# Kernel optimization log

Measured on AMD Instinct MI355X. Metric: run time of the kernel, lower is better.

## Reference

```python
import jax, jax.numpy as jnp
import numpy as np

LN_EPS = 1e-5
MIN_BW, MAX_BW, BW_FACTOR = 0.1, 10.0, 1.0
BETA = 0.1


def _layernorm(h, g, b):
    mu = jnp.mean(h, axis=-1, keepdims=True)
    var = jnp.mean((h - mu) ** 2, axis=-1, keepdims=True)
    return (h - mu) * jax.lax.rsqrt(var + LN_EPS) * g + b


def _mlp(x, W1, b1, g, beta, W2, b2):
    # Linear -> LayerNorm -> Dropout(eval: identity) -> GELU(exact) -> Linear
    h = x @ W1 + b1
    h = _layernorm(h, g, beta)
    h = jax.nn.gelu(h, approximate=False)
    return h @ W2 + b2


def _normalize(x):
    n = jnp.linalg.norm(x, axis=-1, keepdims=True)
    return x / jnp.maximum(n, 1e-12)


def _bandwidth(x, y):
    # median-heuristic bandwidth on up to 512 samples; no grad through it
    s = min(512, x.shape[0])
    xs, ys = x[:s], y[:s]
    diff = xs[:, None, :] - ys[None, :, :]          # [s, s, K]
    dist_sq = jnp.sum(diff ** 2, axis=-1)
    bw = jnp.sqrt(jnp.median(dist_sq.reshape(-1)) / 2.0) * BW_FACTOR
    return jax.lax.stop_gradient(jnp.clip(bw, MIN_BW, MAX_BW))


def _score_kernel(x, sx, y, sy):
    # 3-term KSD kernel matrix [B, B]
    bw = _bandwidth(x, y)
    bw2 = bw ** 2
    x2 = jnp.sum(x ** 2, axis=-1)
    y2 = jnp.sum(y ** 2, axis=-1)
    dist_sq = jnp.maximum(x2[:, None] + y2[None, :] - 2.0 * (x @ y.T), 0.0)
    k = jnp.exp(-dist_sq / (2.0 * bw2))
    term1 = k * (sx @ sy.T)
    # sum_d (x_i - y_j)_d * sy_jd  = x_i . sy_j - y_j . sy_j
    term2 = (x @ sy.T - jnp.sum(y * sy, axis=-1)[None, :]) * k / bw2
    D = x.shape[-1]
    term3 = dist_sq * k / (bw2 ** 2) - k * D / bw2
    return term1 + term2 + term3


def setup_inputs() -> dict:
    key = jax.random.key(0)
    B, L, D1, H, K = 256, 128, 768, 1024, 256
    ks = jax.random.split(key, 16)

    def w(k, shape):
        return (jax.random.normal(k, shape, dtype=jnp.float32) * 0.02)

    inp = {
        'image_features': jax.random.normal(ks[0], (B, L, D1), dtype=jnp.float32),
        'text_features': jax.random.normal(ks[1], (B, L, D1), dtype=jnp.float32),
        'eps_img': jax.random.normal(ks[2], (B, L, K), dtype=jnp.float32),
        'eps_txt': jax.random.normal(ks[3], (B, L, K), dtype=jnp.float32),
        'attention_mask': jnp.ones((B, L), dtype=jnp.int32),
    }
    # encoders: D1 -> H -> 2K ; score nets: K -> 2K -> K
    for pfx, k1, k2 in (('enc_i', ks[4], ks[5]), ('enc_t', ks[6], ks[7])):
        inp[pfx + '_W1'] = w(k1, (D1, H)); inp[pfx + '_b1'] = jnp.zeros((H,), jnp.float32)
        inp[pfx + '_g'] = jnp.ones((H,), jnp.float32); inp[pfx + '_beta'] = jnp.zeros((H,), jnp.float32)
        inp[pfx + '_W2'] = w(k2, (H, 2 * K)); inp[pfx + '_b2'] = jnp.zeros((2 * K,), jnp.float32)
    for pfx, k1, k2 in (('sc_i', ks[8], ks[9]), ('sc_t', ks[10], ks[11])):
        inp[pfx + '_W1'] = w(k1, (K, 2 * K)); inp[pfx + '_b1'] = jnp.zeros((2 * K,), jnp.float32)
        inp[pfx + '_g'] = jnp.ones((2 * K,), jnp.float32); inp[pfx + '_beta'] = jnp.zeros((2 * K,), jnp.float32)
        inp[pfx + '_W2'] = w(k2, (2 * K, K)); inp[pfx + '_b2'] = jnp.zeros((K,), jnp.float32)
    return inp


def reference(image_features, text_features, attention_mask, eps_img, eps_txt,
              enc_i_W1, enc_i_b1, enc_i_g, enc_i_beta, enc_i_W2, enc_i_b2,
              enc_t_W1, enc_t_b1, enc_t_g, enc_t_beta, enc_t_W2, enc_t_b2,
              sc_i_W1, sc_i_b1, sc_i_g, sc_i_beta, sc_i_W2, sc_i_b2,
              sc_t_W1, sc_t_b1, sc_t_g, sc_t_beta, sc_t_W2, sc_t_b2):
    B = image_features.shape[0]
    img_params = _mlp(image_features, enc_i_W1, enc_i_b1, enc_i_g, enc_i_beta, enc_i_W2, enc_i_b2)
    txt_params = _mlp(text_features, enc_t_W1, enc_t_b1, enc_t_g, enc_t_beta, enc_t_W2, enc_t_b2)
    K = img_params.shape[-1] // 2
    img_mu, img_logvar = img_params[..., :K], img_params[..., K:]
    txt_mu, txt_logvar = txt_params[..., :K], txt_params[..., K:]

    img_z = _normalize(img_mu + eps_img * jnp.exp(0.5 * img_logvar))
    txt_z = _normalize(txt_mu + eps_txt * jnp.exp(0.5 * txt_logvar))

    img_score = _mlp(img_z, sc_i_W1, sc_i_b1, sc_i_g, sc_i_beta, sc_i_W2, sc_i_b2)
    txt_score = _mlp(txt_z, sc_t_W1, sc_t_b1, sc_t_g, sc_t_beta, sc_t_W2, sc_t_b2)

    seq_last = jnp.sum(attention_mask, axis=1).astype(jnp.int32) - 1   # [B]
    bidx = jnp.arange(B)
    xz, yz = img_z[bidx, seq_last], txt_z[bidx, seq_last]
    xs, ys = img_score[bidx, seq_last], txt_score[bidx, seq_last]

    alignment_loss = jnp.mean(_score_kernel(xz, xs, yz, ys))

    kl1 = -0.5 * jnp.sum(1.0 + img_logvar - img_mu ** 2 - jnp.exp(img_logvar), axis=-1)
    kl2 = -0.5 * jnp.sum(1.0 + txt_logvar - txt_mu ** 2 - jnp.exp(txt_logvar), axis=-1)
    kl_loss = (jnp.mean(kl1[bidx, seq_last]) + jnp.mean(kl2[bidx, seq_last])) / 2.0

    total_loss = kl_loss + BETA * alignment_loss
    return total_loss
```

## Files before the change

kernel.cpp:

```cpp
#include <hip/hip_runtime.h>
#include <math.h>

#define Bb   256
#define Lq   128
#define D1   768
#define Hh   1024
#define Kk   256
#define K2v  512

#define OFF_EPSG  0
#define OFF_H1    131072
#define OFF_H2    655360
#define OFF_H3    917504
#define OFF_Z     1179648
#define OFF_SCORE 1310720
#define OFF_DIST  1441792
#define OFF_HIST  1507328
#define OFF_SCAL  1515520
#define OFF_YSY   1515528
#define OFF_BF    1516048

#define UB_XG   0
#define UB_WT   393216
#define WT_EW1I 0
#define WT_EW1T 786432
#define WT_EW2I 1572864
#define WT_EW2T 2097152
#define WT_SW1I 2621440
#define WT_SW1T 2752512
#define WT_SW2I 2883584
#define WT_SW2T 3014656

typedef __attribute__((ext_vector_type(8))) short short8v;
typedef __attribute__((ext_vector_type(4))) float f32x4;

__device__ __forceinline__ float wred(float v){
#pragma unroll
  for (int m = 32; m; m >>= 1) v += __shfl_xor(v, m, 64);
  return v;
}
__device__ __forceinline__ int wredi(int v){
#pragma unroll
  for (int m = 32; m; m >>= 1) v += __shfl_xor(v, m, 64);
  return v;
}
__device__ __forceinline__ float gelu_exact(float x){
  return 0.5f * x * (1.0f + erff(x * 0.70710678118654752f));
}
__device__ __forceinline__ ushort f2b(float f){
  union { float f; unsigned u; } v; v.f = f;
  return (ushort)((v.u + 0x7FFFu + ((v.u >> 16) & 1u)) >> 16);
}
__device__ __forceinline__ int swzq(int k8, int m){
  return ((k8 >> 2)*16 + m)*64 + ((((k8 & 3) << 4)) ^ ((m & 3) << 4));
}
__device__ __forceinline__ int swzr(int ks, int l15, int kg){
  return (ks*16 + l15)*64 + ((kg*16) ^ ((l15 & 3) << 4));
}

__device__ __forceinline__ void wconv64(
    const float* __restrict__ src, ushort* __restrict__ dst,
    int Kd, int Nd, int ti, int t, float (*lsf)[65])
{
  const int ntile = Nd >> 6;
  const int k0 = (ti / ntile) << 6, n0 = (ti % ntile) << 6;
  const int r = t >> 2, c4 = t & 3;
  const float4* s4 = reinterpret_cast<const float4*>(src + (size_t)(k0 + r) * Nd + n0);
#pragma unroll
  for (int j = 0; j < 4; j++){
    float4 v = s4[c4 * 4 + j];
    lsf[r][c4*16 + j*4 + 0] = v.x;
    lsf[r][c4*16 + j*4 + 1] = v.y;
    lsf[r][c4*16 + j*4 + 2] = v.z;
    lsf[r][c4*16 + j*4 + 3] = v.w;
  }
  __syncthreads();
  ushort* d = dst + (size_t)(n0 + r) * Kd + k0 + c4 * 16;
#pragma unroll
  for (int h = 0; h < 2; h++){
    short8v o;
#pragma unroll
    for (int j = 0; j < 8; j++) o[j] = (short)f2b(lsf[c4*16 + h*8 + j][r]);
    *reinterpret_cast<short8v*>(d + h*8) = o;
  }
}

__global__ __launch_bounds__(256) void k_prep(
    const float* __restrict__ img, const float* __restrict__ txt,
    const float* __restrict__ epsi, const float* __restrict__ epst,
    const int* __restrict__ mask,
    const float* __restrict__ eW1i, const float* __restrict__ eW1t,
    ushort* __restrict__ xgb, float* __restrict__ epsg, ushort* __restrict__ wt,
    int* __restrict__ ghist, float* __restrict__ scal, float* __restrict__ ysy)
{
  __shared__ __align__(16) float lsf[64][65];
  __shared__ int s_last;
  const int bid = blockIdx.x, t = threadIdx.x;
  if (bid < 256){
    if (t < 8) reinterpret_cast<int4*>(ghist)[bid * 8 + t] = make_int4(0,0,0,0);
    if (bid == 0 && t < 8) scal[t] = 0.0f;
    if (t < 2) ysy[bid * 2 + t] = 0.0f;
    int s = 0;
    if (t < 32){
      int4 v = reinterpret_cast<const int4*>(mask + bid * Lq)[t];
      s = v.x + v.y + v.z + v.w;
    }
    if (t < 64){
      int tot = wredi(s);
      if (t == 0) s_last = tot - 1;
    }
    __syncthreads();
    const int last = s_last;
    if (t < 192){
      float4 v = reinterpret_cast<const float4*>(img + (size_t)(bid*Lq+last)*D1)[t];
      ushort4 o; o.x=f2b(v.x); o.y=f2b(v.y); o.z=f2b(v.z); o.w=f2b(v.w);
      reinterpret_cast<ushort4*>(xgb + (size_t)bid*D1)[t] = o;
      float4 w = reinterpret_cast<const float4*>(txt + (size_t)(bid*Lq+last)*D1)[t];
      ushort4 q; q.x=f2b(w.x); q.y=f2b(w.y); q.z=f2b(w.z); q.w=f2b(w.w);
      reinterpret_cast<ushort4*>(xgb + (size_t)(Bb+bid)*D1)[t] = q;
    }
    if (t < 64){
      reinterpret_cast<float4*>(epsg + (size_t)bid*Kk)[t] =
        reinterpret_cast<const float4*>(epsi + (size_t)(bid*Lq+last)*Kk)[t];
      reinterpret_cast<float4*>(epsg + (size_t)(Bb+bid)*Kk)[t] =
        reinterpret_cast<const float4*>(epst + (size_t)(bid*Lq+last)*Kk)[t];
    }
    return;
  }
  const int wb = bid - 256;
  if (wb < 192) wconv64(eW1i, wt + WT_EW1I, D1, Hh, wb, t, lsf);
  else          wconv64(eW1t, wt + WT_EW1T, D1, Hh, wb - 192, t, lsf);
}

__global__ __launch_bounds__(256) void k_enc1(
    const ushort* __restrict__ xgb,
    const ushort* __restrict__ WTi, const ushort* __restrict__ WTt,
    const float* __restrict__ b1i, const float* __restrict__ b1t,
    const float* __restrict__ eW2i, const float* __restrict__ eW2t,
    ushort* __restrict__ wt, float* __restrict__ H1)
{
  __shared__ __align__(16) char SM[16 * 768 * 2];
  const int bid = blockIdx.x, tid = threadIdx.x;
  if (bid >= 512){
    float (*lsf)[65] = reinterpret_cast<float(*)[65]>(SM);
    const int wb = bid - 512;
    if (wb < 128) wconv64(eW2i, wt + WT_EW2I, Hh, K2v, wb, tid, lsf);
    else          wconv64(eW2t, wt + WT_EW2T, Hh, K2v, wb - 128, tid, lsf);
    return;
  }
  char* ALS = SM;
  const int lane = tid & 63, w = tid >> 6;
  const int r0 = (bid >> 4) * 16, colbase = (bid & 15) * 64;
  const ushort* WT = (r0 >= 256) ? WTt : WTi;
  const float* b1 = (r0 >= 256) ? b1t : b1i;
  const int l15 = lane & 15, kg = lane >> 4;
  const int col = colbase + w*16 + l15;

  short8v areg[6];
  int mA[6], kA[6];
#pragma unroll
  for (int i = 0; i < 6; i++){
    const int q = i*256 + tid;
    mA[i] = q / 96; kA[i] = q % 96;
    areg[i] = *reinterpret_cast<const short8v*>(xgb + (size_t)(r0+mA[i])*D1 + kA[i]*8);
  }
  short8v breg[24];
  const ushort* wp = WT + (size_t)col*D1 + kg*8;
#pragma unroll
  for (int ks = 0; ks < 24; ks++)
    breg[ks] = *reinterpret_cast<const short8v*>(wp + ks*32);
#pragma unroll
  for (int i = 0; i < 6; i++)
    *reinterpret_cast<short8v*>(ALS + swzq(kA[i], mA[i])) = areg[i];
  __syncthreads();
  f32x4 acc = (f32x4){0.f,0.f,0.f,0.f};
#pragma unroll
  for (int ks = 0; ks < 24; ks++){
    short8v av = *reinterpret_cast<const short8v*>(ALS + swzr(ks, l15, kg));
    acc = __builtin_amdgcn_mfma_f32_16x16x32_bf16(av, breg[ks], acc, 0, 0, 0);
  }
  const float bias = b1[col];
#pragma unroll
  for (int r = 0; r < 4; r++)
    H1[(size_t)(r0 + kg*4 + r) * Hh + col] = acc[r] + bias;
}

__global__ __launch_bounds__(512) void k_enc2(
    const float* __restrict__ H1,
    const ushort* __restrict__ WTi, const ushort* __restrict__ WTt,
    const float* __restrict__ gi,  const float* __restrict__ gt,
    const float* __restrict__ bei, const float* __restrict__ bet,
    const float* __restrict__ b2i, const float* __restrict__ b2t,
    const float* __restrict__ sW1i, const float* __restrict__ sW1t,
    const float* __restrict__ sW2i, const float* __restrict__ sW2t,
    ushort* __restrict__ wt, float* __restrict__ H2)
{
  __shared__ __align__(16) char SM[16 * 1024 * 2];
  __shared__ __align__(16) float Rf[4][64][4];
  const int bid = blockIdx.x, tid = threadIdx.x;
  if (bid >= 256){
    if (tid < 256){
      float (*lsf)[65] = reinterpret_cast<float(*)[65]>(SM);
      const int wb = bid - 256;
      if      (wb < 32)  wconv64(sW1i, wt + WT_SW1I, Kk,  K2v, wb,      tid, lsf);
      else if (wb < 64)  wconv64(sW1t, wt + WT_SW1T, Kk,  K2v, wb - 32, tid, lsf);
      else if (wb < 96)  wconv64(sW2i, wt + WT_SW2I, K2v, Kk,  wb - 64, tid, lsf);
      else               wconv64(sW2t, wt + WT_SW2T, K2v, Kk,  wb - 96, tid, lsf);
    }
    return;
  }
  char* ALS = SM;
  const int lane = tid & 63, w = tid >> 6;
  const int r0 = (bid >> 3) * 16, colbase = (bid & 7) * 64;
  const ushort* WT = (r0 >= 256) ? WTt : WTi;
  const float* g  = (r0 >= 256) ? gt  : gi;
  const float* be = (r0 >= 256) ? bet : bei;
  const float* b2 = (r0 >= 256) ? b2t : b2i;
  const int l15 = lane & 15, kg = lane >> 4;
  const int ct = w & 3, khalf = w >> 2;
  const int col = colbase + ct*16 + l15;

  short8v breg[16];
  const ushort* wp = WT + (size_t)col*Hh + khalf*512 + kg*8;
#pragma unroll
  for (int i = 0; i < 16; i++)
    breg[i] = *reinterpret_cast<const short8v*>(wp + i*32);

#pragma unroll
  for (int rr = 0; rr < 2; rr++){
    const int row = w + rr*8, grow = r0 + row;
    const float4* h4 = reinterpret_cast<const float4*>(H1 + (size_t)grow * Hh);
    float4 v0 = h4[lane*4+0], v1 = h4[lane*4+1], v2 = h4[lane*4+2], v3 = h4[lane*4+3];
    float s = v0.x+v0.y+v0.z+v0.w + v1.x+v1.y+v1.z+v1.w
            + v2.x+v2.y+v2.z+v2.w + v3.x+v3.y+v3.z+v3.w;
    float q2 = v0.x*v0.x+v0.y*v0.y+v0.z*v0.z+v0.w*v0.w
             + v1.x*v1.x+v1.y*v1.y+v1.z*v1.z+v1.w*v1.w
             + v2.x*v2.x+v2.y*v2.y+v2.z*v2.z+v2.w*v2.w
             + v3.x*v3.x+v3.y*v3.y+v3.z*v3.z+v3.w*v3.w;
    s = wred(s); q2 = wred(q2);
    const float mean = s * (1.0f/1024.0f);
    const float rstd = rsqrtf(q2 * (1.0f/1024.0f) - mean*mean + 1e-5f);
    const float4* g4  = reinterpret_cast<const float4*>(g);
    const float4* be4 = reinterpret_cast<const float4*>(be);
    float hv[16] = {v0.x,v0.y,v0.z,v0.w, v1.x,v1.y,v1.z,v1.w,
                    v2.x,v2.y,v2.z,v2.w, v3.x,v3.y,v3.z,v3.w};
    short8v o0, o1;
#pragma unroll
    for (int j = 0; j < 16; j++){
      float4 gg = g4[lane*4 + (j>>2)];
      float4 bb = be4[lane*4 + (j>>2)];
      const float gs = (j&3)==0?gg.x:((j&3)==1?gg.y:((j&3)==2?gg.z:gg.w));
      const float bs = (j&3)==0?bb.x:((j&3)==1?bb.y:((j&3)==2?bb.z:bb.w));
      float x = gelu_exact((hv[j] - mean)*rstd*gs + bs);
      if (j < 8) o0[j] = (short)f2b(x); else o1[j-8] = (short)f2b(x);
    }
    *reinterpret_cast<short8v*>(ALS + swzq(lane*2,   row)) = o0;
    *reinterpret_cast<short8v*>(ALS + swzq(lane*2+1, row)) = o1;
  }
  __syncthreads();
  f32x4 acc = (f32x4){0.f,0.f,0.f,0.f};
#pragma unroll
  for (int i = 0; i < 16; i++){
    const int ks = khalf*16 + i;
    short8v av = *reinterpret_cast<const short8v*>(ALS + swzr(ks, l15, kg));
    acc = __builtin_amdgcn_mfma_f32_16x16x32_bf16(av, breg[i], acc, 0, 0, 0);
  }
  if (khalf) *reinterpret_cast<float4*>(&Rf[ct][lane][0]) = make_float4(acc[0],acc[1],acc[2],acc[3]);
  __syncthreads();
  if (!khalf){
    float4 o = *reinterpret_cast<const float4*>(&Rf[ct][lane][0]);
    const float bias = b2[col];
    H2[(size_t)(r0 + kg*4 + 0) * K2v + col] = acc[0]+o.x+bias;
    H2[(size_t)(r0 + kg*4 + 1) * K2v + col] = acc[1]+o.y+bias;
    H2[(size_t)(r0 + kg*4 + 2) * K2v + col] = acc[2]+o.z+bias;
    H2[(size_t)(r0 + kg*4 + 3) * K2v + col] = acc[3]+o.w+bias;
  }
}

__global__ __launch_bounds__(256) void k_sc1(
    const float* __restrict__ H2,
    const float* __restrict__ b2i, const float* __restrict__ b2t,
    const float* __restrict__ epsg,
    const ushort* __restrict__ W1i, const ushort* __restrict__ W1t,
    const float* __restrict__ sb1i, const float* __restrict__ sb1t,
    float* __restrict__ z, float* __restrict__ kl, float* __restrict__ H3)
{
  __shared__ __align__(16) char ALS[16 * 256 * 2];
  const int tid = threadIdx.x, lane = tid & 63, w = tid >> 6;
  const int r0 = blockIdx.y * 16, colblk = blockIdx.x, colbase = colblk * 64;
  const float* b2 = (r0 >= 256) ? b2t : b2i;
  const ushort* W1 = (r0 >= 256) ? W1t : W1i;
  const float* sb1 = (r0 >= 256) ? sb1t : sb1i;
  const int l15 = lane & 15, kg = lane >> 4;
  const int col = colbase + w*16 + l15;

  short8v breg[8];
  const ushort* wp = W1 + (size_t)col*Kk + kg*8;
#pragma unroll
  for (int ks = 0; ks < 8; ks++)
    breg[ks] = *reinterpret_cast<const short8v*>(wp + ks*32);

#pragma unroll
  for (int rr = 0; rr < 4; rr++){
    const int row = w + rr*4, grow = r0 + row;
    const float4* h4 = reinterpret_cast<const float4*>(H2 + (size_t)grow * K2v);
    float4 mu = h4[lane], lv = h4[64 + lane];
    float4 bm = reinterpret_cast<const float4*>(b2)[lane];
    float4 bl = reinterpret_cast<const float4*>(b2)[64 + lane];
    mu.x += bm.x; mu.y += bm.y; mu.z += bm.z; mu.w += bm.w;
    lv.x += bl.x; lv.y += bl.y; lv.z += bl.z; lv.w += bl.w;
    float4 ev = reinterpret_cast<const float4*>(epsg)[(size_t)grow * 64 + lane];
    float z0 = mu.x + ev.x * expf(0.5f * lv.x);
    float z1 = mu.y + ev.y * expf(0.5f * lv.y);
    float z2 = mu.z + ev.z * expf(0.5f * lv.z);
    float z3 = mu.w + ev.w * expf(0.5f * lv.w);
    float s2 = wred(z0*z0 + z1*z1 + z2*z2 + z3*z3);
    float klp = (1.0f + lv.x - mu.x*mu.x - expf(lv.x))
              + (1.0f + lv.y - mu.y*mu.y - expf(lv.y))
              + (1.0f + lv.z - mu.z*mu.z - expf(lv.z))
              + (1.0f + lv.w - mu.w*mu.w - expf(lv.w));
    float klt = wred(klp);
    float inv = 1.0f / fmaxf(sqrtf(s2), 1e-12f);
    float4 zv = make_float4(z0*inv, z1*inv, z2*inv, z3*inv);
    if (colblk == 0){
      reinterpret_cast<float4*>(z)[(size_t)grow * 64 + lane] = zv;
      if (lane == 0) atomicAdd(kl + (grow >= 256 ? 1 : 0), -0.5f * klt);
    }
    ushort4 o; o.x=f2b(zv.x); o.y=f2b(zv.y); o.z=f2b(zv.z); o.w=f2b(zv.w);
    *reinterpret_cast<ushort4*>(ALS + swzq(lane >> 1, row) + (lane & 1)*8) = o;
  }
  __syncthreads();
  f32x4 acc = (f32x4){0.f,0.f,0.f,0.f};
#pragma unroll
  for (int ks = 0; ks < 8; ks++){
    short8v av = *reinterpret_cast<const short8v*>(ALS + swzr(ks, l15, kg));
    acc = __builtin_amdgcn_mfma_f32_16x16x32_bf16(av, breg[ks], acc, 0, 0, 0);
  }
  const float bias = sb1[col];
#pragma unroll
  for (int r = 0; r < 4; r++)
    H3[(size_t)(r0 + kg*4 + r) * K2v + col] = acc[r] + bias;
}

__global__ __launch_bounds__(256) void k_sc2(
    const float* __restrict__ H3,
    const float* __restrict__ sgi,  const float* __restrict__ sgt,
    const float* __restrict__ sbei, const float* __restrict__ sbet,
    const ushort* __restrict__ W2i, const ushort* __restrict__ W2t,
    const float* __restrict__ sb2i, const float* __restrict__ sb2t,
    const float* __restrict__ z, float* __restrict__ score, float* __restrict__ ysy,
    float* __restrict__ dist, int* __restrict__ ghist)
{
  __shared__ __align__(16) char SM[33792];
  const int bid = blockIdx.x, tid = threadIdx.x;
  if (bid < 128){
    char* ALS = SM;
    const int lane = tid & 63, w = tid >> 6;
    const int r0 = (bid >> 2) * 16, colbase = (bid & 3) * 64;
    const float* g  = (r0 >= 256) ? sgt  : sgi;
    const float* be = (r0 >= 256) ? sbet : sbei;
    const ushort* W2 = (r0 >= 256) ? W2t : W2i;
    const float* b2 = (r0 >= 256) ? sb2t : sb2i;
    const int l15 = lane & 15, kg = lane >> 4;
    const int col = colbase + w*16 + l15;

    short8v breg[16];
    const ushort* wp = W2 + (size_t)col*K2v + kg*8;
#pragma unroll
    for (int ks = 0; ks < 16; ks++)
      breg[ks] = *reinterpret_cast<const short8v*>(wp + ks*32);

#pragma unroll
    for (int rr = 0; rr < 4; rr++){
      const int row = w + rr*4, grow = r0 + row;
      const float4* h4 = reinterpret_cast<const float4*>(H3 + (size_t)grow * K2v);
      float4 a = h4[lane*2], b = h4[lane*2+1];
      float s = a.x+a.y+a.z+a.w + b.x+b.y+b.z+b.w;
      float q2 = a.x*a.x+a.y*a.y+a.z*a.z+a.w*a.w + b.x*b.x+b.y*b.y+b.z*b.z+b.w*b.w;
      s = wred(s); q2 = wred(q2);
      const float mean = s * (1.0f/512.0f);
      const float rstd = rsqrtf(q2 * (1.0f/512.0f) - mean*mean + 1e-5f);
      float4 g0 = reinterpret_cast<const float4*>(g)[lane*2];
      float4 g1 = reinterpret_cast<const float4*>(g)[lane*2+1];
      float4 e0 = reinterpret_cast<const float4*>(be)[lane*2];
      float4 e1 = reinterpret_cast<const float4*>(be)[lane*2+1];
      short8v o;
      o[0] = (short)f2b(gelu_exact((a.x-mean)*rstd*g0.x + e0.x));
      o[1] = (short)f2b(gelu_exact((a.y-mean)*rstd*g0.y + e0.y));
      o[2] = (short)f2b(gelu_exact((a.z-mean)*rstd*g0.z + e0.z));
      o[3] = (short)f2b(gelu_exact((a.w-mean)*rstd*g0.w + e0.w));
      o[4] = (short)f2b(gelu_exact((b.x-mean)*rstd*g1.x + e1.x));
      o[5] = (short)f2b(gelu_exact((b.y-mean)*rstd*g1.y + e1.y));
      o[6] = (short)f2b(gelu_exact((b.z-mean)*rstd*g1.z + e1.z));
      o[7] = (short)f2b(gelu_exact((b.w-mean)*rstd*g1.w + e1.w));
      *reinterpret_cast<short8v*>(ALS + swzq(lane, row)) = o;
    }
    __syncthreads();
    f32x4 acc = (f32x4){0.f,0.f,0.f,0.f};
#pragma unroll
    for (int ks = 0; ks < 16; ks++){
      short8v av = *reinterpret_cast<const short8v*>(ALS + swzr(ks, l15, kg));
      acc = __builtin_amdgcn_mfma_f32_16x16x32_bf16(av, breg[ks], acc, 0, 0, 0);
    }
    const float bias = b2[col];
    float part[4];
#pragma unroll
    for (int r = 0; r < 4; r++){
      const int grow = r0 + kg*4 + r;
      const float sv = acc[r] + bias;
      score[(size_t)grow * Kk + col] = sv;
      part[r] = z[(size_t)grow * Kk + col] * sv;
    }
#pragma unroll
    for (int m = 1; m < 16; m <<= 1){
#pragma unroll
      for (int r = 0; r < 4; r++) part[r] += __shfl_xor(part[r], m, 64);
    }
    if (l15 == 0){
#pragma unroll
      for (int r = 0; r < 4; r++) atomicAdd(&ysy[r0 + kg*4 + r], part[r]);
    }
    return;
  }
  float* xsh = reinterpret_cast<float*>(SM);
  int* hl = reinterpret_cast<int*>(SM + 1024);
  const int i = bid - 128, j = tid;
  xsh[j] = z[(size_t)i * Kk + j];
  for (int k = j; k < 8192; k += 256) hl[k] = 0;
  __syncthreads();
  const float4* y4 = reinterpret_cast<const float4*>(z + (size_t)Bb * Kk);
  const float4* x4 = reinterpret_cast<const float4*>(xsh);
  float acc = 0.0f;
#pragma unroll 8
  for (int d = 0; d < Kk; d += 4){
    float4 xv = x4[d >> 2];
    float4 yv = y4[j * (Kk/4) + (d >> 2)];
    float d0 = xv.x - yv.x, d1 = xv.y - yv.y, d2 = xv.z - yv.z, d3 = xv.w - yv.w;
    acc += d0*d0 + d1*d1 + d2*d2 + d3*d3;
  }
  dist[i * 256 + j] = acc;
  int bin = (int)(acc * 2048.0f);
  bin = bin < 0 ? 0 : (bin > 8191 ? 8191 : bin);
  atomicAdd(&hl[bin], 1);
  __syncthreads();
  for (int k = j; k < 8192; k += 256){
    int c = hl[k];
    if (c) atomicAdd(ghist + k, c);
  }
}

__global__ __launch_bounds__(256) void k_score(
    const float* __restrict__ z, const float* __restrict__ score,
    const float* __restrict__ dist, const float* __restrict__ ysy,
    const int* __restrict__ ghist, float* __restrict__ scal,
    float* __restrict__ out)
{
  __shared__ __align__(16) float xsh[Kk];
  __shared__ __align__(16) float sxsh[Kk];
  __shared__ int wt4[4];
  __shared__ int bres[2];
  __shared__ float red4[4];
  __shared__ float s_bw2;
  const int i = blockIdx.x, j = threadIdx.x;
  xsh[j]  = z[(size_t)i * Kk + j];
  sxsh[j] = score[(size_t)i * Kk + j];
  {
    const int lane = j & 63, w = j >> 6;
    const int base = j * 32;
    int s = 0;
#pragma unroll
    for (int u = 0; u < 32; u++) s += ghist[base + u];
    int sc = s;
#pragma unroll
    for (int m = 1; m < 64; m <<= 1){
      int o = __shfl_up(sc, m, 64);
      if (lane >= m) sc += o;
    }
    if (lane == 63) wt4[w] = sc;
    __syncthreads();
    int off = 0;
    for (int q = 0; q < w; q++) off += wt4[q];
    int cum = sc + off, basex = cum - s;
#pragma unroll
    for (int rr = 0; rr < 2; rr++){
      int rank = 32768 + rr;
      if (basex < rank && cum >= rank){
        int c = basex;
        for (int u = 0; u < 32; u++){
          c += ghist[base + u];
          if (c >= rank){ bres[rr] = base + u; break; }
        }
      }
    }
    __syncthreads();
    if (j == 0){
      float med = 0.5f * ((bres[0] + 0.5f) + (bres[1] + 0.5f)) * (1.0f / 2048.0f);
      float bw = sqrtf(med * 0.5f);
      bw = fminf(fmaxf(bw, 0.1f), 10.0f);
      s_bw2 = bw * bw;
    }
    __syncthreads();
  }
  const float bw2 = s_bw2;
  const float4* sy4 = reinterpret_cast<const float4*>(score + (size_t)Bb * Kk);
  const float4* x4  = reinterpret_cast<const float4*>(xsh);
  const float4* sx4 = reinterpret_cast<const float4*>(sxsh);
  float ssy = 0, xsy = 0;
#pragma unroll 8
  for (int d = 0; d < Kk; d += 4){
    float4 xv  = x4[d >> 2];
    float4 sxv = sx4[d >> 2];
    float4 syv = sy4[j * (Kk/4) + (d >> 2)];
    ssy += sxv.x*syv.x + sxv.y*syv.y + sxv.z*syv.z + sxv.w*syv.w;
    xsy += xv.x*syv.x + xv.y*syv.y + xv.z*syv.z + xv.w*syv.w;
  }
  float d2 = dist[i * 256 + j];
  float kv = expf(-d2 / (2.0f * bw2));
  float t1 = kv * ssy;
  float t2 = (xsy - ysy[Bb + j]) * kv / bw2;
  float t3 = d2 * kv / (bw2 * bw2) - kv * (float)Kk / bw2;
  float s = wred(t1 + t2 + t3);
  if (!(j & 63)) red4[j >> 6] = s;
  __syncthreads();
  if (j == 0){
    atomicAdd(scal + 2, red4[0] + red4[1] + red4[2] + red4[3]);
    __threadfence();
    int old = atomicAdd(reinterpret_cast<int*>(scal + 4), 1);
    if (old == 255){
      float kli = __int_as_float(atomicAdd(reinterpret_cast<int*>(scal + 0), 0));
      float klt = __int_as_float(atomicAdd(reinterpret_cast<int*>(scal + 1), 0));
      float alg = __int_as_float(atomicAdd(reinterpret_cast<int*>(scal + 2), 0));
      out[0] = 0.5f * (kli + klt) * (1.0f/256.0f) + 0.1f * alg * (1.0f/65536.0f);
    }
  }
}

extern "C" void kernel_launch(void* const* d_in, const int* in_sizes, int n_in,
                              void* d_out, int out_size, void* d_ws, size_t ws_size,
                              hipStream_t stream) {
  (void)in_sizes; (void)n_in; (void)out_size; (void)ws_size;
  const float* img  = (const float*)d_in[0];
  const float* txt  = (const float*)d_in[1];
  const float* epsi = (const float*)d_in[2];
  const float* epst = (const float*)d_in[3];
  const int*   mask = (const int*)d_in[4];
  const float* eW1i = (const float*)d_in[5];
  const float* eb1i = (const float*)d_in[6];
  const float* egi  = (const float*)d_in[7];
  const float* ebei = (const float*)d_in[8];
  const float* eW2i = (const float*)d_in[9];
  const float* eb2i = (const float*)d_in[10];
  const float* eW1t = (const float*)d_in[11];
  const float* eb1t = (const float*)d_in[12];
  const float* egt  = (const float*)d_in[13];
  const float* ebet = (const float*)d_in[14];
  const float* eW2t = (const float*)d_in[15];
  const float* eb2t = (const float*)d_in[16];
  const float* sW1i = (const float*)d_in[17];
  const float* sb1i = (const float*)d_in[18];
  const float* sgi  = (const float*)d_in[19];
  const float* sbei = (const float*)d_in[20];
  const float* sW2i = (const float*)d_in[21];
  const float* sb2i = (const float*)d_in[22];
  const float* sW1t = (const float*)d_in[23];
  const float* sb1t = (const float*)d_in[24];
  const float* sgt  = (const float*)d_in[25];
  const float* sbet = (const float*)d_in[26];
  const float* sW2t = (const float*)d_in[27];
  const float* sb2t = (const float*)d_in[28];

  float*  ws    = (float*)d_ws;
  float*  epsg  = ws + OFF_EPSG;
  float*  H1    = ws + OFF_H1;
  float*  H2    = ws + OFF_H2;
  float*  H3    = ws + OFF_H3;
  float*  z     = ws + OFF_Z;
  float*  score = ws + OFF_SCORE;
  float*  dist  = ws + OFF_DIST;
  int*    ghist = (int*)(ws + OFF_HIST);
  float*  scal  = ws + OFF_SCAL;
  float*  ysy   = ws + OFF_YSY;
  ushort* ub    = (ushort*)(ws + OFF_BF);
  ushort* xgb   = ub + UB_XG;
  ushort* wt    = ub + UB_WT;

  k_prep<<<640, 256, 0, stream>>>(img, txt, epsi, epst, mask,
                                  eW1i, eW1t, xgb, epsg, wt, ghist, scal, ysy);
  k_enc1<<<768, 256, 0, stream>>>(xgb, wt+WT_EW1I, wt+WT_EW1T, eb1i, eb1t,
                                  eW2i, eW2t, wt, H1);
  k_enc2<<<384, 512, 0, stream>>>(H1, wt+WT_EW2I, wt+WT_EW2T,
                                  egi, egt, ebei, ebet, eb2i, eb2t,
                                  sW1i, sW1t, sW2i, sW2t, wt, H2);
  k_sc1<<<dim3(8, 32), 256, 0, stream>>>(H2, eb2i, eb2t, epsg,
                                         wt+WT_SW1I, wt+WT_SW1T, sb1i, sb1t,
                                         z, scal, H3);
  k_sc2<<<384, 256, 0, stream>>>(H3, sgi, sgt, sbei, sbet,
                                 wt+WT_SW2I, wt+WT_SW2T, sb2i, sb2t,
                                 z, score, ysy, dist, ghist);
  k_score<<<256, 256, 0, stream>>>(z, score, dist, ysy, ghist, scal, (float*)d_out);
}
```

Baseline: 88.02 us.

## Merge six kernels into three using global flag-based inter-block dependencies

Moves all weight bf16 conversions into the prep kernel. It fuses enc1 with enc2, and sc1, sc2 and score into single launches, where dependent blocks spin on global atomic counters per row group instead of waiting at kernel boundaries. The goal is to remove launch gaps and tail idle time between the small stages. The risks are deadlock if waiting blocks occupy the CUs before their producers are scheduled, spin-polling overhead, and the loss of the split-K parallelism that enc2 had.

```diff
diff --git a/kernel.cpp b/kernel.cpp
--- a/kernel.cpp
+++ b/kernel.cpp
@@ -19,6 +19,7 @@
 #define OFF_SCAL  1515520
 #define OFF_YSY   1515528
 #define OFF_BF    1516048
+#define OFF_FLAGS 3285520
 
 #define UB_XG   0
 #define UB_WT   393216
@@ -57,6 +58,17 @@
 __device__ __forceinline__ int swzr(int ks, int l15, int kg){
   return (ks*16 + l15)*64 + ((kg*16) ^ ((l15 & 3) << 4));
 }
+__device__ __forceinline__ void postflag(int* f, int tid){
+  __syncthreads();
+  if (tid == 0){ __threadfence(); atomicAdd(f, 1); }
+}
+__device__ __forceinline__ void waitflag(int* f, int target, int tid){
+  if (tid == 0){
+    while (atomicAdd(f, 0) < target) __builtin_amdgcn_s_sleep(8);
+    __threadfence();
+  }
+  __syncthreads();
+}
 
 __device__ __forceinline__ void wconv64(
     const float* __restrict__ src, ushort* __restrict__ dst,
@@ -90,8 +102,11 @@
     const float* __restrict__ epsi, const float* __restrict__ epst,
     const int* __restrict__ mask,
     const float* __restrict__ eW1i, const float* __restrict__ eW1t,
+    const float* __restrict__ eW2i, const float* __restrict__ eW2t,
+    const float* __restrict__ sW1i, const float* __restrict__ sW1t,
+    const float* __restrict__ sW2i, const float* __restrict__ sW2t,
     ushort* __restrict__ xgb, float* __restrict__ epsg, ushort* __restrict__ wt,
-    int* __restrict__ ghist, float* __restrict__ scal, float* __restrict__ ysy)
+    int* ghist, float* scal, float* ysy, int* flags)
 {
   __shared__ __align__(16) float lsf[64][65];
   __shared__ int s_last;
@@ -99,6 +114,7 @@
   if (bid < 256){
     if (t < 8) reinterpret_cast<int4*>(ghist)[bid * 8 + t] = make_int4(0,0,0,0);
     if (bid == 0 && t < 8) scal[t] = 0.0f;
+    if (bid == 1 && t < 128) flags[t] = 0;
     if (t < 2) ysy[bid * 2 + t] = 0.0f;
     int s = 0;
     if (t < 32){
@@ -127,108 +143,108 @@
     }
     return;
   }
-  const int wb = bid - 256;
-  if (wb < 192) wconv64(eW1i, wt + WT_EW1I, D1, Hh, wb, t, lsf);
-  else          wconv64(eW1t, wt + WT_EW1T, D1, Hh, wb - 192, t, lsf);
-}
-
-__global__ __launch_bounds__(256) void k_enc1(
+  int wb = bid - 256;
+  if (wb < 384){
+    if (wb < 192) wconv64(eW1i, wt + WT_EW1I, D1, Hh, wb, t, lsf);
+    else          wconv64(eW1t, wt + WT_EW1T, D1, Hh, wb - 192, t, lsf);
+    return;
+  }
+  wb -= 384;
+  if (wb < 256){
+    if (wb < 128) wconv64(eW2i, wt + WT_EW2I, Hh, K2v, wb, t, lsf);
+    else          wconv64(eW2t, wt + WT_EW2T, Hh, K2v, wb - 128, t, lsf);
+    return;
+  }
+  wb -= 256;
+  if (wb < 64){
+    if (wb < 32) wconv64(sW1i, wt + WT_SW1I, Kk, K2v, wb, t, lsf);
+    else         wconv64(sW1t, wt + WT_SW1T, Kk, K2v, wb - 32, t, lsf);
+    return;
+  }
+  wb -= 64;
+  if (wb < 32) wconv64(sW2i, wt + WT_SW2I, K2v, Kk, wb, t, lsf);
+  else         wconv64(sW2t, wt + WT_SW2T, K2v, Kk, wb - 32, t, lsf);
+}
+
+__global__ __launch_bounds__(256) void k_fuse1(
     const ushort* __restrict__ xgb,
-    const ushort* __restrict__ WTi, const ushort* __restrict__ WTt,
+    const ushort* __restrict__ wte1i, const ushort* __restrict__ wte1t,
+    const ushort* __restrict__ wte2i, const ushort* __restrict__ wte2t,
     const float* __restrict__ b1i, const float* __restrict__ b1t,
-    const float* __restrict__ eW2i, const float* __restrict__ eW2t,
-    ushort* __restrict__ wt, float* __restrict__ H1)
-{
-  __shared__ __align__(16) char SM[16 * 768 * 2];
-  const int bid = blockIdx.x, tid = threadIdx.x;
-  if (bid >= 512){
-    float (*lsf)[65] = reinterpret_cast<float(*)[65]>(SM);
-    const int wb = bid - 512;
-    if (wb < 128) wconv64(eW2i, wt + WT_EW2I, Hh, K2v, wb, tid, lsf);
-    else          wconv64(eW2t, wt + WT_EW2T, Hh, K2v, wb - 128, tid, lsf);
-    return;
-  }
-  char* ALS = SM;
-  const int lane = tid & 63, w = tid >> 6;
-  const int r0 = (bid >> 4) * 16, colbase = (bid & 15) * 64;
-  const ushort* WT = (r0 >= 256) ? WTt : WTi;
-  const float* b1 = (r0 >= 256) ? b1t : b1i;
-  const int l15 = lane & 15, kg = lane >> 4;
-  const int col = colbase + w*16 + l15;
-
-  short8v areg[6];
-  int mA[6], kA[6];
-#pragma unroll
-  for (int i = 0; i < 6; i++){
-    const int q = i*256 + tid;
-    mA[i] = q / 96; kA[i] = q % 96;
-    areg[i] = *reinterpret_cast<const short8v*>(xgb + (size_t)(r0+mA[i])*D1 + kA[i]*8);
-  }
-  short8v breg[24];
-  const ushort* wp = WT + (size_t)col*D1 + kg*8;
-#pragma unroll
-  for (int ks = 0; ks < 24; ks++)
-    breg[ks] = *reinterpret_cast<const short8v*>(wp + ks*32);
-#pragma unroll
-  for (int i = 0; i < 6; i++)
-    *reinterpret_cast<short8v*>(ALS + swzq(kA[i], mA[i])) = areg[i];
-  __syncthreads();
-  f32x4 acc = (f32x4){0.f,0.f,0.f,0.f};
-#pragma unroll
-  for (int ks = 0; ks < 24; ks++){
-    short8v av = *reinterpret_cast<const short8v*>(ALS + swzr(ks, l15, kg));
-    acc = __builtin_amdgcn_mfma_f32_16x16x32_bf16(av, breg[ks], acc, 0, 0, 0);
-  }
-  const float bias = b1[col];
-#pragma unroll
-  for (int r = 0; r < 4; r++)
-    H1[(size_t)(r0 + kg*4 + r) * Hh + col] = acc[r] + bias;
-}
-
-__global__ __launch_bounds__(512) void k_enc2(
-    const float* __restrict__ H1,
-    const ushort* __restrict__ WTi, const ushort* __restrict__ WTt,
     const float* __restrict__ gi,  const float* __restrict__ gt,
     const float* __restrict__ bei, const float* __restrict__ bet,
     const float* __restrict__ b2i, const float* __restrict__ b2t,
-    const float* __restrict__ sW1i, const float* __restrict__ sW1t,
-    const float* __restrict__ sW2i, const float* __restrict__ sW2t,
-    ushort* __restrict__ wt, float* __restrict__ H2)
+    float* H1, float* H2, int* flags)
 {
-  __shared__ __align__(16) char SM[16 * 1024 * 2];
-  __shared__ __align__(16) float Rf[4][64][4];
+  __shared__ __align__(16) char SM[32768];
   const int bid = blockIdx.x, tid = threadIdx.x;
-  if (bid >= 256){
-    if (tid < 256){
-      float (*lsf)[65] = reinterpret_cast<float(*)[65]>(SM);
-      const int wb = bid - 256;
-      if      (wb < 32)  wconv64(sW1i, wt + WT_SW1I, Kk,  K2v, wb,      tid, lsf);
-      else if (wb < 64)  wconv64(sW1t, wt + WT_SW1T, Kk,  K2v, wb - 32, tid, lsf);
-      else if (wb < 96)  wconv64(sW2i, wt + WT_SW2I, K2v, Kk,  wb - 64, tid, lsf);
-      else               wconv64(sW2t, wt + WT_SW2T, K2v, Kk,  wb - 96, tid, lsf);
-    }
-    return;
-  }
+  const int lane = tid & 63, w = tid >> 6;
+  const int l15 = lane & 15, kg = lane >> 4;
   char* ALS = SM;
-  const int lane = tid & 63, w = tid >> 6;
-  const int r0 = (bid >> 3) * 16, colbase = (bid & 7) * 64;
-  const ushort* WT = (r0 >= 256) ? WTt : WTi;
+  if (bid < 512){
+    const int rg = bid >> 4;
+    const int r0 = rg * 16, colbase = (bid & 15) * 64;
+    const ushort* WT = (r0 >= 256) ? wte1t : wte1i;
+    const float* b1 = (r0 >= 256) ? b1t : b1i;
+    const int col = colbase + w*16 + l15;
+    short8v areg[6]; int mA[6], kA[6];
+#pragma unroll
+    for (int i = 0; i < 6; i++){
+      const int q = i*256 + tid;
+      mA[i] = q / 96; kA[i] = q % 96;
+      areg[i] = *reinterpret_cast<const short8v*>(xgb + (size_t)(r0+mA[i])*D1 + kA[i]*8);
+    }
+    const ushort* wp = WT + (size_t)col*D1 + kg*8;
+    short8v ba[8], bb[8];
+#pragma unroll
+    for (int i = 0; i < 8; i++) ba[i] = *reinterpret_cast<const short8v*>(wp + i*32);
+#pragma unroll
+    for (int i = 0; i < 6; i++)
+      *reinterpret_cast<short8v*>(ALS + swzq(kA[i], mA[i])) = areg[i];
+    __syncthreads();
+    f32x4 acc = (f32x4){0.f,0.f,0.f,0.f};
+#pragma unroll
+    for (int i = 0; i < 8; i++) bb[i] = *reinterpret_cast<const short8v*>(wp + (8+i)*32);
+#pragma unroll
+    for (int i = 0; i < 8; i++){
+      short8v av = *reinterpret_cast<const short8v*>(ALS + swzr(i, l15, kg));
+      acc = __builtin_amdgcn_mfma_f32_16x16x32_bf16(av, ba[i], acc, 0, 0, 0);
+    }
+#pragma unroll
+    for (int i = 0; i < 8; i++) ba[i] = *reinterpret_cast<const short8v*>(wp + (16+i)*32);
+#pragma unroll
+    for (int i = 0; i < 8; i++){
+      short8v av = *reinterpret_cast<const short8v*>(ALS + swzr(8+i, l15, kg));
+      acc = __builtin_amdgcn_mfma_f32_16x16x32_bf16(av, bb[i], acc, 0, 0, 0);
+    }
+#pragma unroll
+    for (int i = 0; i < 8; i++){
+      short8v av = *reinterpret_cast<const short8v*>(ALS + swzr(16+i, l15, kg));
+      acc = __builtin_amdgcn_mfma_f32_16x16x32_bf16(av, ba[i], acc, 0, 0, 0);
+    }
+    const float bias = b1[col];
+#pragma unroll
+    for (int r = 0; r < 4; r++)
+      H1[(size_t)(r0 + kg*4 + r) * Hh + col] = acc[r] + bias;
+    postflag(flags + rg, tid);
+    return;
+  }
+  const int b2id = bid - 512;
+  const int rg = b2id >> 3;
+  const int r0 = rg * 16, colbase = (b2id & 7) * 64;
+  const ushort* WT = (r0 >= 256) ? wte2t : wte2i;
   const float* g  = (r0 >= 256) ? gt  : gi;
   const float* be = (r0 >= 256) ? bet : bei;
   const float* b2 = (r0 >= 256) ? b2t : b2i;
-  const int l15 = lane & 15, kg = lane >> 4;
-  const int ct = w & 3, khalf = w >> 2;
-  const int col = colbase + ct*16 + l15;
-
-  short8v breg[16];
-  const ushort* wp = WT + (size_t)col*Hh + khalf*512 + kg*8;
-#pragma unroll
-  for (int i = 0; i < 16; i++)
-    breg[i] = *reinterpret_cast<const short8v*>(wp + i*32);
-
-#pragma unroll
-  for (int rr = 0; rr < 2; rr++){
-    const int row = w + rr*8, grow = r0 + row;
+  const int col = colbase + w*16 + l15;
+  waitflag(flags + rg, 16, tid);
+  const ushort* wp = WT + (size_t)col*Hh + kg*8;
+  short8v ba[8], bb[8];
+#pragma unroll
+  for (int i = 0; i < 8; i++) ba[i] = *reinterpret_cast<const short8v*>(wp + i*32);
+#pragma unroll
+  for (int rr = 0; rr < 4; rr++){
+    const int row = w + rr*4, grow = r0 + row;
     const float4* h4 = reinterpret_cast<const float4*>(H1 + (size_t)grow * Hh);
     float4 v0 = h4[lane*4+0], v1 = h4[lane*4+1], v2 = h4[lane*4+2], v3 = h4[lane*4+3];
     float s = v0.x+v0.y+v0.z+v0.w + v1.x+v1.y+v1.z+v1.w
@@ -248,9 +264,9 @@
 #pragma unroll
     for (int j = 0; j < 16; j++){
       float4 gg = g4[lane*4 + (j>>2)];
-      float4 bb = be4[lane*4 + (j>>2)];
+      float4 bbv = be4[lane*4 + (j>>2)];
       const float gs = (j&3)==0?gg.x:((j&3)==1?gg.y:((j&3)==2?gg.z:gg.w));
-      const float bs = (j&3)==0?bb.x:((j&3)==1?bb.y:((j&3)==2?bb.z:bb.w));
+      const float bs = (j&3)==0?bbv.x:((j&3)==1?bbv.y:((j&3)==2?bbv.z:bbv.w));
       float x = gelu_exact((hv[j] - mean)*rstd*gs + bs);
       if (j < 8) o0[j] = (short)f2b(x); else o1[j-8] = (short)f2b(x);
     }
@@ -260,116 +276,131 @@
   __syncthreads();
   f32x4 acc = (f32x4){0.f,0.f,0.f,0.f};
 #pragma unroll
-  for (int i = 0; i < 16; i++){
-    const int ks = khalf*16 + i;
-    short8v av = *reinterpret_cast<const short8v*>(ALS + swzr(ks, l15, kg));
-    acc = __builtin_amdgcn_mfma_f32_16x16x32_bf16(av, breg[i], acc, 0, 0, 0);
-  }
-  if (khalf) *reinterpret_cast<float4*>(&Rf[ct][lane][0]) = make_float4(acc[0],acc[1],acc[2],acc[3]);
-  __syncthreads();
-  if (!khalf){
-    float4 o = *reinterpret_cast<const float4*>(&Rf[ct][lane][0]);
-    const float bias = b2[col];
-    H2[(size_t)(r0 + kg*4 + 0) * K2v + col] = acc[0]+o.x+bias;
-    H2[(size_t)(r0 + kg*4 + 1) * K2v + col] = acc[1]+o.y+bias;
-    H2[(size_t)(r0 + kg*4 + 2) * K2v + col] = acc[2]+o.z+bias;
-    H2[(size_t)(r0 + kg*4 + 3) * K2v + col] = acc[3]+o.w+bias;
-  }
-}
-
-__global__ __launch_bounds__(256) void k_sc1(
-    const float* __restrict__ H2,
+  for (int i = 0; i < 8; i++) bb[i] = *reinterpret_cast<const short8v*>(wp + (8+i)*32);
+#pragma unroll
+  for (int i = 0; i < 8; i++){
+    short8v av = *reinterpret_cast<const short8v*>(ALS + swzr(i, l15, kg));
+    acc = __builtin_amdgcn_mfma_f32_16x16x32_bf16(av, ba[i], acc, 0, 0, 0);
+  }
+#pragma unroll
+  for (int i = 0; i < 8; i++) ba[i] = *reinterpret_cast<const short8v*>(wp + (16+i)*32);
+#pragma unroll
+  for (int i = 0; i < 8; i++){
+    short8v av = *reinterpret_cast<const short8v*>(ALS + swzr(8+i, l15, kg));
+    acc = __builtin_amdgcn_mfma_f32_16x16x32_bf16(av, bb[i], acc, 0, 0, 0);
+  }
+#pragma unroll
+  for (int i = 0; i < 8; i++) bb[i] = *reinterpret_cast<const short8v*>(wp + (24+i)*32);
+#pragma unroll
+  for (int i = 0; i < 8; i++){
+    short8v av = *reinterpret_cast<const short8v*>(ALS + swzr(16+i, l15, kg));
+    acc = __builtin_amdgcn_mfma_f32_16x16x32_bf16(av, ba[i], acc, 0, 0, 0);
+  }
+#pragma unroll
+  for (int i = 0; i < 8; i++){
+    short8v av = *reinterpret_cast<const short8v*>(ALS + swzr(24+i, l15, kg));
+    acc = __builtin_amdgcn_mfma_f32_16x16x32_bf16(av, bb[i], acc, 0, 0, 0);
+  }
+  const float bias = b2[col];
+#pragma unroll
+  for (int r = 0; r < 4; r++)
+    H2[(size_t)(r0 + kg*4 + r) * K2v + col] = acc[r] + bias;
+}
+
+__global__ __launch_bounds__(256) void k_fuse2(
+    const float* H2,
     const float* __restrict__ b2i, const float* __restrict__ b2t,
     const float* __restrict__ epsg,
     const ushort* __restrict__ W1i, const ushort* __restrict__ W1t,
     const float* __restrict__ sb1i, const float* __restrict__ sb1t,
-    float* __restrict__ z, float* __restrict__ kl, float* __restrict__ H3)
-{
-  __shared__ __align__(16) char ALS[16 * 256 * 2];
-  const int tid = threadIdx.x, lane = tid & 63, w = tid >> 6;
-  const int r0 = blockIdx.y * 16, colblk = blockIdx.x, colbase = colblk * 64;
-  const float* b2 = (r0 >= 256) ? b2t : b2i;
-  const ushort* W1 = (r0 >= 256) ? W1t : W1i;
-  const float* sb1 = (r0 >= 256) ? sb1t : sb1i;
-  const int l15 = lane & 15, kg = lane >> 4;
-  const int col = colbase + w*16 + l15;
-
-  short8v breg[8];
-  const ushort* wp = W1 + (size_t)col*Kk + kg*8;
-#pragma unroll
-  for (int ks = 0; ks < 8; ks++)
-    breg[ks] = *reinterpret_cast<const short8v*>(wp + ks*32);
-
-#pragma unroll
-  for (int rr = 0; rr < 4; rr++){
-    const int row = w + rr*4, grow = r0 + row;
-    const float4* h4 = reinterpret_cast<const float4*>(H2 + (size_t)grow * K2v);
-    float4 mu = h4[lane], lv = h4[64 + lane];
-    float4 bm = reinterpret_cast<const float4*>(b2)[lane];
-    float4 bl = reinterpret_cast<const float4*>(b2)[64 + lane];
-    mu.x += bm.x; mu.y += bm.y; mu.z += bm.z; mu.w += bm.w;
-    lv.x += bl.x; lv.y += bl.y; lv.z += bl.z; lv.w += bl.w;
-    float4 ev = reinterpret_cast<const float4*>(epsg)[(size_t)grow * 64 + lane];
-    float z0 = mu.x + ev.x * expf(0.5f * lv.x);
-    float z1 = mu.y + ev.y * expf(0.5f * lv.y);
-    float z2 = mu.z + ev.z * expf(0.5f * lv.z);
-    float z3 = mu.w + ev.w * expf(0.5f * lv.w);
-    float s2 = wred(z0*z0 + z1*z1 + z2*z2 + z3*z3);
-    float klp = (1.0f + lv.x - mu.x*mu.x - expf(lv.x))
-              + (1.0f + lv.y - mu.y*mu.y - expf(lv.y))
-              + (1.0f + lv.z - mu.z*mu.z - expf(lv.z))
-              + (1.0f + lv.w - mu.w*mu.w - expf(lv.w));
-    float klt = wred(klp);
-    float inv = 1.0f / fmaxf(sqrtf(s2), 1e-12f);
-    float4 zv = make_float4(z0*inv, z1*inv, z2*inv, z3*inv);
-    if (colblk == 0){
-      reinterpret_cast<float4*>(z)[(size_t)grow * 64 + lane] = zv;
-      if (lane == 0) atomicAdd(kl + (grow >= 256 ? 1 : 0), -0.5f * klt);
-    }
-    ushort4 o; o.x=f2b(zv.x); o.y=f2b(zv.y); o.z=f2b(zv.z); o.w=f2b(zv.w);
-    *reinterpret_cast<ushort4*>(ALS + swzq(lane >> 1, row) + (lane & 1)*8) = o;
-  }
-  __syncthreads();
-  f32x4 acc = (f32x4){0.f,0.f,0.f,0.f};
-#pragma unroll
-  for (int ks = 0; ks < 8; ks++){
-    short8v av = *reinterpret_cast<const short8v*>(ALS + swzr(ks, l15, kg));
-    acc = __builtin_amdgcn_mfma_f32_16x16x32_bf16(av, breg[ks], acc, 0, 0, 0);
-  }
-  const float bias = sb1[col];
-#pragma unroll
-  for (int r = 0; r < 4; r++)
-    H3[(size_t)(r0 + kg*4 + r) * K2v + col] = acc[r] + bias;
-}
-
-__global__ __launch_bounds__(256) void k_sc2(
-    const float* __restrict__ H3,
     const float* __restrict__ sgi,  const float* __restrict__ sgt,
     const float* __restrict__ sbei, const float* __restrict__ sbet,
     const ushort* __restrict__ W2i, const ushort* __restrict__ W2t,
     const float* __restrict__ sb2i, const float* __restrict__ sb2t,
-    const float* __restrict__ z, float* __restrict__ score, float* __restrict__ ysy,
-    float* __restrict__ dist, int* __restrict__ ghist)
+    float* z, float* H3, float* score, float* ysy,
+    float* dist, int* ghist, float* scal, float* out, int* flags)
 {
   __shared__ __align__(16) char SM[33792];
   const int bid = blockIdx.x, tid = threadIdx.x;
-  if (bid < 128){
+  const int lane = tid & 63, w = tid >> 6;
+  const int l15 = lane & 15, kg = lane >> 4;
+  if (bid < 256){
     char* ALS = SM;
-    const int lane = tid & 63, w = tid >> 6;
-    const int r0 = (bid >> 2) * 16, colbase = (bid & 3) * 64;
+    const int rg = bid >> 3, cb = bid & 7;
+    const int r0 = rg * 16, colbase = cb * 64;
+    const float* b2 = (r0 >= 256) ? b2t : b2i;
+    const ushort* W1 = (r0 >= 256) ? W1t : W1i;
+    const float* sb1 = (r0 >= 256) ? sb1t : sb1i;
+    const int col = colbase + w*16 + l15;
+    short8v breg[8];
+    const ushort* wp = W1 + (size_t)col*Kk + kg*8;
+#pragma unroll
+    for (int ks = 0; ks < 8; ks++)
+      breg[ks] = *reinterpret_cast<const short8v*>(wp + ks*32);
+#pragma unroll
+    for (int rr = 0; rr < 4; rr++){
+      const int row = w + rr*4, grow = r0 + row;
+      const float4* h4 = reinterpret_cast<const float4*>(H2 + (size_t)grow * K2v);
+      float4 mu = h4[lane], lv = h4[64 + lane];
+      float4 bm = reinterpret_cast<const float4*>(b2)[lane];
+      float4 bl = reinterpret_cast<const float4*>(b2)[64 + lane];
+      mu.x += bm.x; mu.y += bm.y; mu.z += bm.z; mu.w += bm.w;
+      lv.x += bl.x; lv.y += bl.y; lv.z += bl.z; lv.w += bl.w;
+      float4 ev = reinterpret_cast<const float4*>(epsg)[(size_t)grow * 64 + lane];
+      float z0 = mu.x + ev.x * expf(0.5f * lv.x);
+      float z1 = mu.y + ev.y * expf(0.5f * lv.y);
+      float z2 = mu.z + ev.z * expf(0.5f * lv.z);
+      float z3 = mu.w + ev.w * expf(0.5f * lv.w);
+      float s2 = wred(z0*z0 + z1*z1 + z2*z2 + z3*z3);
+      float klp = (1.0f + lv.x - mu.x*mu.x - expf(lv.x))
+                + (1.0f + lv.y - mu.y*mu.y - expf(lv.y))
+                + (1.0f + lv.z - mu.z*mu.z - expf(lv.z))
+                + (1.0f + lv.w - mu.w*mu.w - expf(lv.w));
+      float klt = wred(klp);
+      float inv = 1.0f / fmaxf(sqrtf(s2), 1e-12f);
+      float4 zv = make_float4(z0*inv, z1*inv, z2*inv, z3*inv);
+      if (cb == 0){
+        reinterpret_cast<float4*>(z)[(size_t)grow * 64 + lane] = zv;
+        if (lane == 0) atomicAdd(scal + (grow >= 256 ? 1 : 0), -0.5f * klt);
+      }
+      ushort4 o; o.x=f2b(zv.x); o.y=f2b(zv.y); o.z=f2b(zv.z); o.w=f2b(zv.w);
+      *reinterpret_cast<ushort4*>(ALS + swzq(lane >> 1, row) + (lane & 1)*8) = o;
+    }
+    __syncthreads();
+    f32x4 acc = (f32x4){0.f,0.f,0.f,0.f};
+#pragma unroll
+    for (int ks = 0; ks < 8; ks++){
+      short8v av = *reinterpret_cast<const short8v*>(ALS + swzr(ks, l15, kg));
+      acc = __builtin_amdgcn_mfma_f32_16x16x32_bf16(av, breg[ks], acc, 0, 0, 0);
+    }
+    const float bias = sb1[col];
+#pragma unroll
+    for (int r = 0; r < 4; r++)
+      H3[(size_t)(r0 + kg*4 + r) * K2v + col] = acc[r] + bias;
+    __syncthreads();
+    if (tid == 0){
+      __threadfence();
+      atomicAdd(flags + 32 + rg, 1);
+      if (cb == 0) atomicAdd(flags + 64, 1);
+    }
+    return;
+  }
+  if (bid < 384){
+    char* ALS = SM;
+    const int b2id = bid - 256;
+    const int rg = b2id >> 2;
+    const int r0 = rg * 16, colbase = (b2id & 3) * 64;
     const float* g  = (r0 >= 256) ? sgt  : sgi;
     const float* be = (r0 >= 256) ? sbet : sbei;
     const ushort* W2 = (r0 >= 256) ? W2t : W2i;
     const float* b2 = (r0 >= 256) ? sb2t : sb2i;
-    const int l15 = lane & 15, kg = lane >> 4;
     const int col = colbase + w*16 + l15;
-
+    waitflag(flags + 32 + rg, 8, tid);
     short8v breg[16];
     const ushort* wp = W2 + (size_t)col*K2v + kg*8;
 #pragma unroll
     for (int ks = 0; ks < 16; ks++)
       breg[ks] = *reinterpret_cast<const short8v*>(wp + ks*32);
-
 #pragma unroll
     for (int rr = 0; rr < 4; rr++){
       const int row = w + rr*4, grow = r0 + row;
@@ -420,117 +451,123 @@
 #pragma unroll
       for (int r = 0; r < 4; r++) atomicAdd(&ysy[r0 + kg*4 + r], part[r]);
     }
-    return;
-  }
-  float* xsh = reinterpret_cast<float*>(SM);
-  int* hl = reinterpret_cast<int*>(SM + 1024);
-  const int i = bid - 128, j = tid;
-  xsh[j] = z[(size_t)i * Kk + j];
-  for (int k = j; k < 8192; k += 256) hl[k] = 0;
-  __syncthreads();
-  const float4* y4 = reinterpret_cast<const float4*>(z + (size_t)Bb * Kk);
-  const float4* x4 = reinterpret_cast<const float4*>(xsh);
-  float acc = 0.0f;
+    postflag(flags + 66, tid);
+    return;
+  }
+  if (bid < 640){
+    float* xsh = reinterpret_cast<float*>(SM);
+    int* hl = reinterpret_cast<int*>(SM + 1024);
+    const int i = bid - 384, j = tid;
+    waitflag(flags + 64, 32, tid);
+    xsh[j] = z[(size_t)i * Kk + j];
+    for (int k = j; k < 8192; k += 256) hl[k] = 0;
+    __syncthreads();
+    const float4* y4 = reinterpret_cast<const float4*>(z + (size_t)Bb * Kk);
+    const float4* x4 = reinterpret_cast<const float4*>(xsh);
+    float acc = 0.0f;
 #pragma unroll 8
-  for (int d = 0; d < Kk; d += 4){
-    float4 xv = x4[d >> 2];
-    float4 yv = y4[j * (Kk/4) + (d >> 2)];
-    float d0 = xv.x - yv.x, d1 = xv.y - yv.y, d2 = xv.z - yv.z, d3 = xv.w - yv.w;
-    acc += d0*d0 + d1*d1 + d2*d2 + d3*d3;
-  }
-  dist[i * 256 + j] = acc;
-  int bin = (int)(acc * 2048.0f);
-  bin = bin < 0 ? 0 : (bin > 8191 ? 8191 : bin);
-  atomicAdd(&hl[bin], 1);
-  __syncthreads();
-  for (int k = j; k < 8192; k += 256){
-    int c = hl[k];
-    if (c) atomicAdd(ghist + k, c);
-  }
-}
-
-__global__ __launch_bounds__(256) void k_score(
-    const float* __restrict__ z, const float* __restrict__ score,
-    const float* __restrict__ dist, const float* __restrict__ ysy,
-    const int* __restrict__ ghist, float* __restrict__ scal,
-    float* __restrict__ out)
-{
-  __shared__ __align__(16) float xsh[Kk];
-  __shared__ __align__(16) float sxsh[Kk];
-  __shared__ int wt4[4];
-  __shared__ int bres[2];
-  __shared__ float red4[4];
-  __shared__ float s_bw2;
-  const int i = blockIdx.x, j = threadIdx.x;
-  xsh[j]  = z[(size_t)i * Kk + j];
-  sxsh[j] = score[(size_t)i * Kk + j];
+    for (int d = 0; d < Kk; d += 4){
+      float4 xv = x4[d >> 2];
+      float4 yv = y4[j * (Kk/4) + (d >> 2)];
+      float d0 = xv.x - yv.x, d1 = xv.y - yv.y, d2 = xv.z - yv.z, d3 = xv.w - yv.w;
+      acc += d0*d0 + d1*d1 + d2*d2 + d3*d3;
+    }
+    dist[i * 256 + j] = acc;
+    int bin = (int)(acc * 2048.0f);
+    bin = bin < 0 ? 0 : (bin > 8191 ? 8191 : bin);
+    atomicAdd(&hl[bin], 1);
+    __syncthreads();
+    for (int k = j; k < 8192; k += 256){
+      int c = hl[k];
+      if (c) atomicAdd(ghist + k, c);
+    }
+    postflag(flags + 65, tid);
+    return;
+  }
   {
-    const int lane = j & 63, w = j >> 6;
-    const int base = j * 32;
-    int s = 0;
-#pragma unroll
-    for (int u = 0; u < 32; u++) s += ghist[base + u];
-    int sc = s;
-#pragma unroll
-    for (int m = 1; m < 64; m <<= 1){
-      int o = __shfl_up(sc, m, 64);
-      if (lane >= m) sc += o;
-    }
-    if (lane == 63) wt4[w] = sc;
-    __syncthreads();
-    int off = 0;
-    for (int q = 0; q < w; q++) off += wt4[q];
-    int cum = sc + off, basex = cum - s;
-#pragma unroll
-    for (int rr = 0; rr < 2; rr++){
-      int rank = 32768 + rr;
-      if (basex < rank && cum >= rank){
-        int c = basex;
-        for (int u = 0; u < 32; u++){
-          c += ghist[base + u];
-          if (c >= rank){ bres[rr] = base + u; break; }
+    float* xsh  = reinterpret_cast<float*>(SM);
+    float* sxsh = reinterpret_cast<float*>(SM + 1024);
+    int* wt4  = reinterpret_cast<int*>(SM + 2048);
+    int* bres = reinterpret_cast<int*>(SM + 2064);
+    float* red4 = reinterpret_cast<float*>(SM + 2080);
+    float* s_bw2 = reinterpret_cast<float*>(SM + 2096);
+    const int i = bid - 640, j = tid;
+    if (j == 0){
+      while (atomicAdd(flags + 65, 0) < 256 || atomicAdd(flags + 66, 0) < 128)
+        __builtin_amdgcn_s_sleep(8);
+      __threadfence();
+    }
+    __syncthreads();
+    xsh[j]  = z[(size_t)i * Kk + j];
+    sxsh[j] = score[(size_t)i * Kk + j];
+    {
+      const int lane6 = j & 63, wv = j >> 6;
+      const int base = j * 32;
+      int s = 0;
+#pragma unroll
+      for (int u = 0; u < 32; u++) s += ghist[base + u];
+      int sc = s;
+#pragma unroll
+      for (int m = 1; m < 64; m <<= 1){
+        int o = __shfl_up(sc, m, 64);
+        if (lane6 >= m) sc += o;
+      }
+      if (lane6 == 63) wt4[wv] = sc;
+      __syncthreads();
+      int off = 0;
+      for (int q = 0; q < wv; q++) off += wt4[q];
+      int cum = sc + off, basex = cum - s;
+#pragma unroll
+      for (int rr = 0; rr < 2; rr++){
+        int rank = 32768 + rr;
+        if (basex < rank && cum >= rank){
+          int c = basex;
+          for (int u = 0; u < 32; u++){
+            c += ghist[base + u];
+            if (c >= rank){ bres[rr] = base + u; break; }
+          }
         }
       }
-    }
+      __syncthreads();
+      if (j == 0){
+        float med = 0.5f * ((bres[0] + 0.5f) + (bres[1] + 0.5f)) * (1.0f / 2048.0f);
+        float bw = sqrtf(med * 0.5f);
+        bw = fminf(fmaxf(bw, 0.1f), 10.0f);
+        s_bw2[0] = bw * bw;
+      }
+      __syncthreads();
+    }
+    const float bw2 = s_bw2[0];
+    const float4* sy4 = reinterpret_cast<const float4*>(score + (size_t)Bb * Kk);
+    const float4* x4  = reinterpret_cast<const float4*>(xsh);
+    const float4* sx4 = reinterpret_cast<const float4*>(sxsh);
+    float ssy = 0, xsy = 0;
+#pragma unroll 8
+    for (int d = 0; d < Kk; d += 4){
+      float4 xv  = x4[d >> 2];
+      float4 sxv = sx4[d >> 2];
+      float4 syv = sy4[j * (Kk/4) + (d >> 2)];
+      ssy += sxv.x*syv.x + sxv.y*syv.y + sxv.z*syv.z + sxv.w*syv.w;
+      xsy += xv.x*syv.x + xv.y*syv.y + xv.z*syv.z + xv.w*syv.w;
+    }
+    float d2 = dist[i * 256 + j];
+    float kv = expf(-d2 / (2.0f * bw2));
+    float t1 = kv * ssy;
+    float t2 = (xsy - ysy[Bb + j]) * kv / bw2;
+    float t3 = d2 * kv / (bw2 * bw2) - kv * (float)Kk / bw2;
+    float s = wred(t1 + t2 + t3);
+    if (!(j & 63)) red4[j >> 6] = s;
     __syncthreads();
     if (j == 0){
-      float med = 0.5f * ((bres[0] + 0.5f) + (bres[1] + 0.5f)) * (1.0f / 2048.0f);
-      float bw = sqrtf(med * 0.5f);
-      bw = fminf(fmaxf(bw, 0.1f), 10.0f);
-      s_bw2 = bw * bw;
-    }
-    __syncthreads();
-  }
-  const float bw2 = s_bw2;
-  const float4* sy4 = reinterpret_cast<const float4*>(score + (size_t)Bb * Kk);
-  const float4* x4  = reinterpret_cast<const float4*>(xsh);
-  const float4* sx4 = reinterpret_cast<const float4*>(sxsh);
-  float ssy = 0, xsy = 0;
-#pragma unroll 8
-  for (int d = 0; d < Kk; d += 4){
-    float4 xv  = x4[d >> 2];
-    float4 sxv = sx4[d >> 2];
-    float4 syv = sy4[j * (Kk/4) + (d >> 2)];
-    ssy += sxv.x*syv.x + sxv.y*syv.y + sxv.z*syv.z + sxv.w*syv.w;
-    xsy += xv.x*syv.x + xv.y*syv.y + xv.z*syv.z + xv.w*syv.w;
-  }
-  float d2 = dist[i * 256 + j];
-  float kv = expf(-d2 / (2.0f * bw2));
-  float t1 = kv * ssy;
-  float t2 = (xsy - ysy[Bb + j]) * kv / bw2;
-  float t3 = d2 * kv / (bw2 * bw2) - kv * (float)Kk / bw2;
-  float s = wred(t1 + t2 + t3);
-  if (!(j & 63)) red4[j >> 6] = s;
-  __syncthreads();
-  if (j == 0){
-    atomicAdd(scal + 2, red4[0] + red4[1] + red4[2] + red4[3]);
-    __threadfence();
-    int old = atomicAdd(reinterpret_cast<int*>(scal + 4), 1);
-    if (old == 255){
-      float kli = __int_as_float(atomicAdd(reinterpret_cast<int*>(scal + 0), 0));
-      float klt = __int_as_float(atomicAdd(reinterpret_cast<int*>(scal + 1), 0));
-      float alg = __int_as_float(atomicAdd(reinterpret_cast<int*>(scal + 2), 0));
-      out[0] = 0.5f * (kli + klt) * (1.0f/256.0f) + 0.1f * alg * (1.0f/65536.0f);
+      atomicAdd(scal + 2, red4[0] + red4[1] + red4[2] + red4[3]);
+      __threadfence();
+      int old = atomicAdd(reinterpret_cast<int*>(scal + 4), 1);
+      if (old == 255){
+        float kli = __int_as_float(atomicAdd(reinterpret_cast<int*>(scal + 0), 0));
+        float klt = __int_as_float(atomicAdd(reinterpret_cast<int*>(scal + 1), 0));
+        float alg = __int_as_float(atomicAdd(reinterpret_cast<int*>(scal + 2), 0));
+        out[0] = 0.5f * (kli + klt) * (1.0f/256.0f) + 0.1f * alg * (1.0f/65536.0f);
+      }
     }
   }
 }
@@ -580,22 +617,23 @@
   int*    ghist = (int*)(ws + OFF_HIST);
   float*  scal  = ws + OFF_SCAL;
   float*  ysy   = ws + OFF_YSY;
+  int*    flags = (int*)(ws + OFF_FLAGS);
   ushort* ub    = (ushort*)(ws + OFF_BF);
   ushort* xgb   = ub + UB_XG;
   ushort* wt    = ub + UB_WT;
 
-  k_prep<<<640, 256, 0, stream>>>(img, txt, epsi, epst, mask,
-                                  eW1i, eW1t, xgb, epsg, wt, ghist, scal, ysy);
-  k_enc1<<<768, 256, 0, stream>>>(xgb, wt+WT_EW1I, wt+WT_EW1T, eb1i, eb1t,
-                                  eW2i, eW2t, wt, H1);
-  k_enc2<<<384, 512, 0, stream>>>(H1, wt+WT_EW2I, wt+WT_EW2T,
-                                  egi, egt, ebei, ebet, eb2i, eb2t,
-                                  sW1i, sW1t, sW2i, sW2t, wt, H2);
-  k_sc1<<<dim3(8, 32), 256, 0, stream>>>(H2, eb2i, eb2t, epsg,
-                                         wt+WT_SW1I, wt+WT_SW1T, sb1i, sb1t,
-                                         z, scal, H3);
-  k_sc2<<<384, 256, 0, stream>>>(H3, sgi, sgt, sbei, sbet,
-                                 wt+WT_SW2I, wt+WT_SW2T, sb2i, sb2t,
-                                 z, score, ysy, dist, ghist);
-  k_score<<<256, 256, 0, stream>>>(z, score, dist, ysy, ghist, scal, (float*)d_out);
-}
+  k_prep<<<1024, 256, 0, stream>>>(img, txt, epsi, epst, mask,
+                                   eW1i, eW1t, eW2i, eW2t,
+                                   sW1i, sW1t, sW2i, sW2t,
+                                   xgb, epsg, wt, ghist, scal, ysy, flags);
+  k_fuse1<<<768, 256, 0, stream>>>(xgb, wt+WT_EW1I, wt+WT_EW1T,
+                                   wt+WT_EW2I, wt+WT_EW2T,
+                                   eb1i, eb1t, egi, egt, ebei, ebet,
+                                   eb2i, eb2t, H1, H2, flags);
+  k_fuse2<<<896, 256, 0, stream>>>(H2, eb2i, eb2t, epsg,
+                                   wt+WT_SW1I, wt+WT_SW1T, sb1i, sb1t,
+                                   sgi, sgt, sbei, sbet,
+                                   wt+WT_SW2I, wt+WT_SW2T, sb2i, sb2t,
+                                   z, H3, score, ysy, dist, ghist, scal,
+                                   (float*)d_out, flags);
+}
```

Result: slower. 192.1 us (+118.2%).
